# Kernel optimization log

Measured on AMD Instinct MI355X. Metric: run time of the kernel, lower is better.

## Reference

```python
import jax, jax.numpy as jnp
import numpy as np

N, E, H, L, IN, OUT = 50000, 800000, 64, 14, 128, 112
MSG_EPS = 1e-7   # GENConv message epsilon
LN_EPS = 1e-5    # torch.nn.LayerNorm default eps


def setup_inputs() -> dict:
    key = jax.random.key(0)
    ks = jax.random.split(key, 8)
    s = 0.05
    x = jax.random.normal(ks[0], (N, IN), jnp.float32)
    edge_index = jax.random.randint(ks[1], (2, E), 0, N, dtype=jnp.int64)
    enc_W = jax.random.normal(ks[2], (IN, H), jnp.float32) * s
    enc_b = jnp.zeros((H,), jnp.float32)
    ln_g = jnp.ones((L, H), jnp.float32)
    ln_b = jnp.zeros((L, H), jnp.float32)
    mlp_W = jax.random.normal(ks[3], (L, H, H), jnp.float32) * s
    mlp_b = jnp.zeros((L, H), jnp.float32)
    pred_W = jax.random.normal(ks[4], (H, OUT), jnp.float32) * s
    pred_b = jnp.zeros((OUT,), jnp.float32)
    return dict(x=x, edge_index=edge_index, enc_W=enc_W, enc_b=enc_b,
                ln_g=ln_g, ln_b=ln_b, mlp_W=mlp_W, mlp_b=mlp_b,
                pred_W=pred_W, pred_b=pred_b)


def _layernorm(h, g, b):
    mu = jnp.mean(h, axis=-1, keepdims=True)
    var = jnp.mean(jnp.square(h - mu), axis=-1, keepdims=True)  # biased, as torch
    return (h - mu) * jax.lax.rsqrt(var + LN_EPS) * g + b


def _genconv(h, src, dst, W, b):
    # GENConv: msg = relu(x_src) + eps; softmax aggregation (t=1) over dst; out = Linear(x + agg)
    msg = jax.nn.relu(h[src]) + MSG_EPS                    # [E, H]
    mmax = jax.ops.segment_max(msg, dst, num_segments=N)   # [N, H]
    mmax = jnp.where(jnp.isfinite(mmax), mmax, 0.0)         # empty segments
    ex = jnp.exp(msg - mmax[dst])                           # [E, H]
    denom = jax.ops.segment_sum(ex, dst, num_segments=N)    # [N, H]
    num = jax.ops.segment_sum(msg * ex, dst, num_segments=N)
    agg = num / jnp.maximum(denom, 1e-16)                   # 0 for isolated nodes
    return (h + agg) @ W + b


def reference(x, edge_index, enc_W, enc_b, ln_g, ln_b, mlp_W, mlp_b, pred_W, pred_b):
    src, dst = edge_index[0], edge_index[1]
    h = x @ enc_W + enc_b                       # node feature encoder
    h = _genconv(h, src, dst, mlp_W[0], mlp_b[0])  # first GCN (no pre-norm in res+)

    def body(h, params):
        g, bl, W, b = params
        h2 = jax.nn.relu(_layernorm(h, g, bl))  # dropout is identity (eval)
        h = _genconv(h2, src, dst, W, b) + h    # residual
        return h, None

    h, _ = jax.lax.scan(body, h, (ln_g[:L - 1], ln_b[:L - 1], mlp_W[1:], mlp_b[1:]))
    return h @ pred_W + pred_b
```

## Files before the change

kernel.cpp:

```cpp
#include <hip/hip_runtime.h>
#include <hip/hip_bf16.h>

#define NN 50000
#define EE 800000
#define HD 64
#define LL 14
#define IND 128
#define OUTD 112
#define LN2 0.69314718056f

typedef __attribute__((ext_vector_type(8))) short short8;
typedef __attribute__((ext_vector_type(4))) float float4_;
typedef __attribute__((ext_vector_type(4))) unsigned short ushort4_;

__device__ __forceinline__ short bf16_hi(float x) {
    return (short)(__float_as_uint(x) >> 16);
}
__device__ __forceinline__ float bf16_f(short s) {
    return __uint_as_float(((unsigned)(unsigned short)s) << 16);
}
__device__ __forceinline__ float us2f(unsigned u) {
    return __uint_as_float(u << 16);
}
__device__ __forceinline__ unsigned short f2b_rne(float x) {
    unsigned u = __float_as_uint(x);
    u += 0x7fffu + ((u >> 16) & 1u);
    return (unsigned short)(u >> 16);
}

__device__ __forceinline__ void split8(const float* p, short8& hi, short8& lo) {
    float4_ a = *(const float4_*)p;
    float4_ b = *(const float4_*)(p + 4);
    float v[8] = {a[0], a[1], a[2], a[3], b[0], b[1], b[2], b[3]};
    #pragma unroll
    for (int j = 0; j < 8; ++j) {
        short h = bf16_hi(v[j]);
        hi[j] = h;
        lo[j] = bf16_hi(v[j] - bf16_f(h));
    }
}

__device__ __forceinline__ void load_b(const float* __restrict__ W, int ldw,
                                       int colbase, int krow, short8& hi, short8& lo) {
    #pragma unroll
    for (int j = 0; j < 8; ++j) {
        float wv = W[(krow + j) * ldw + colbase];
        short h = bf16_hi(wv);
        hi[j] = h;
        lo[j] = bf16_hi(wv - bf16_f(h));
    }
}

__device__ __forceinline__ float4_ mm3(short8 ah, short8 al, short8 bh, short8 bl,
                                       float4_ acc) {
    acc = __builtin_amdgcn_mfma_f32_16x16x32_bf16(ah, bh, acc, 0, 0, 0);
    acc = __builtin_amdgcn_mfma_f32_16x16x32_bf16(al, bh, acc, 0, 0, 0);
    acc = __builtin_amdgcn_mfma_f32_16x16x32_bf16(ah, bl, acc, 0, 0, 0);
    return acc;
}


__global__ void k_hist(const int* __restrict__ ei, int* __restrict__ cnt,
                       int* __restrict__ rank) {
    int e = blockIdx.x * blockDim.x + threadIdx.x;
    if (e < EE) rank[e] = atomicAdd(&cnt[ei[EE + e]], 1);
}

__global__ __launch_bounds__(1024) void k_scan1(const int* __restrict__ deg,
                                                int* __restrict__ excl,
                                                int* __restrict__ bsum) {
    __shared__ int ws[16];
    int tid = threadIdx.x, lane = tid & 63, w = tid >> 6;
    int gid = blockIdx.x * 1024 + tid;
    int v = (gid < NN) ? deg[gid] : 0;
    int x = v;
    #pragma unroll
    for (int d = 1; d < 64; d <<= 1) {
        int y = __shfl_up(x, d);
        if (lane >= d) x += y;
    }
    if (lane == 63) ws[w] = x;
    __syncthreads();
    if (tid == 0) {
        int acc = 0;
        for (int i = 0; i < 16; i++) { int t = ws[i]; ws[i] = acc; acc += t; }
        bsum[blockIdx.x] = acc;
    }
    __syncthreads();
    if (gid < NN) excl[gid] = x - v + ws[w];
}

__global__ void k_scan2(const int* __restrict__ bsum, int* __restrict__ boff, int nb) {
    int lane = threadIdx.x & 63;
    int v = (lane < nb) ? bsum[lane] : 0;
    int x = v;
    #pragma unroll
    for (int d = 1; d < 64; d <<= 1) {
        int y = __shfl_up(x, d);
        if (lane >= d) x += y;
    }
    if (lane < nb) boff[lane] = x - v;
}

__global__ __launch_bounds__(1024) void k_scan3(int* __restrict__ rp,
                                                const int* __restrict__ boff) {
    int gid = blockIdx.x * 1024 + threadIdx.x;
    if (gid < NN) rp[gid] += boff[blockIdx.x];
    if (gid == 0) rp[NN] = EE;
}

__global__ void k_scatter(const int* __restrict__ ei, const int* __restrict__ rp,
                          const int* __restrict__ rank, int* __restrict__ csrc) {
    int e = blockIdx.x * blockDim.x + threadIdx.x;
    if (e < EE) {
        int d = ei[EE + e];
        csrc[rp[d] + rank[e]] = ei[e];
    }
}


__global__ __launch_bounds__(256) void k_enc(const float* __restrict__ x,
                                             const float* __restrict__ W,
                                             const float* __restrict__ b,
                                             float* __restrict__ h,
                                             unsigned short* __restrict__ P0) {
    __shared__ float X[16 * 132];
    int tid = threadIdx.x, lane = tid & 63, w = tid >> 6;
    int nb = blockIdx.x * 16;
    int nq = lane >> 4, nr = lane & 15;
    int colbase = w * 16 + nr;

    {
        const float* src = x + (size_t)nb * IND + tid * 8;
        float4_ a = *(const float4_*)src;
        float4_ c = *(const float4_*)(src + 4);
        int m = tid >> 4, k8 = 8 * (tid & 15);
        *(float4_*)&X[m * 132 + k8] = a;
        *(float4_*)&X[m * 132 + k8 + 4] = c;
    }
    __syncthreads();

    float4_ acc = {};
    #pragma unroll
    for (int t = 0; t < 4; ++t) {
        short8 ah, al, bh, bl;
        split8(&X[nr * 132 + t * 32 + nq * 8], ah, al);
        load_b(W, HD, colbase, t * 32 + nq * 8, bh, bl);
        acc = mm3(ah, al, bh, bl, acc);
    }

    float bias = b[colbase];
    #pragma unroll
    for (int r = 0; r < 4; ++r) {
        int node = nb + nq * 4 + r;
        float y = acc[r] + bias;
        h[node * HD + colbase] = y;
        float msg = fminf(fmaxf(y, 0.f) + 1e-7f, 50.f);
        P0[node * HD + colbase] = f2b_rne(__expf(msg));
    }
}


__global__ __launch_bounds__(256) void k_gather(const unsigned short* __restrict__ Pin,
                                                const float* __restrict__ selfh,
                                                float* __restrict__ gT,
                                                const int* __restrict__ rp,
                                                const int* __restrict__ csrc) {
    int w = threadIdx.x >> 6, lane = threadIdx.x & 63;
    int node = blockIdx.x * 4 + w;
    int beg = rp[node], deg = rp[node + 1] - beg;

    float s = 0.f, n = 0.f;
    for (int chunk = 0; chunk < deg; chunk += 64) {
        int cnt = min(64, deg - chunk);
        int my = (lane < cnt) ? csrc[beg + chunk + lane] : 0;
        int e = 0;
        for (; e + 4 <= cnt; e += 4) {
            int s0 = __shfl(my, e + 0);
            int s1 = __shfl(my, e + 1);
            int s2 = __shfl(my, e + 2);
            int s3 = __shfl(my, e + 3);
            float p0 = us2f(Pin[s0 * HD + lane]);
            float p1 = us2f(Pin[s1 * HD + lane]);
            float p2 = us2f(Pin[s2 * HD + lane]);
            float p3 = us2f(Pin[s3 * HD + lane]);
            n = fmaf(p0, LN2 * __log2f(p0), n); s += p0;
            n = fmaf(p1, LN2 * __log2f(p1), n); s += p1;
            n = fmaf(p2, LN2 * __log2f(p2), n); s += p2;
            n = fmaf(p3, LN2 * __log2f(p3), n); s += p3;
        }
        for (; e < cnt; ++e) {
            int sr = __shfl(my, e);
            float p = us2f(Pin[sr * HD + lane]);
            n = fmaf(p, LN2 * __log2f(p), n); s += p;
        }
    }
    float agg = n / fmaxf(s, 1e-16f);

    float self;
    if (selfh) {
        self = selfh[(size_t)node * HD + lane];
    } else {
        float ps = us2f(Pin[(size_t)node * HD + lane]);
        self = LN2 * __log2f(ps) - 1e-7f;
    }
    gT[(size_t)node * HD + lane] = self + agg;
}


__global__ __launch_bounds__(256) void k_mm(const float* __restrict__ gT,
                                            const float* __restrict__ hres,
                                            float* __restrict__ hout,
                                            unsigned short* __restrict__ Pout,
                                            const float* __restrict__ W,
                                            const float* __restrict__ b,
                                            const float* __restrict__ gnext,
                                            const float* __restrict__ bnext) {
    __shared__ float T[16 * 68];
    int tid = threadIdx.x, lane = tid & 63, w = tid >> 6;
    int nb = blockIdx.x * 16;
    int nq = lane >> 4, nr = lane & 15;
    int colbase = w * 16 + nr;

    {
        const float* src = gT + (size_t)nb * HD + tid * 4;
        float4_ a = *(const float4_*)src;
        int m = tid >> 4, k4 = 4 * (tid & 15);
        *(float4_*)&T[m * 68 + k4] = a;
    }
    __syncthreads();

    short8 Ahi[2], Alo[2];
    #pragma unroll
    for (int t = 0; t < 2; ++t)
        split8(&T[nr * 68 + t * 32 + nq * 8], Ahi[t], Alo[t]);
    __syncthreads();

    float4_ acc = {};
    #pragma unroll
    for (int t = 0; t < 2; ++t) {
        short8 bh, bl;
        load_b(W, HD, colbase, t * 32 + nq * 8, bh, bl);
        acc = mm3(Ahi[t], Alo[t], bh, bl, acc);
    }

    float bias = b[colbase];
    #pragma unroll
    for (int r = 0; r < 4; ++r) {
        int m = nq * 4 + r;
        int node = nb + m;
        float v = acc[r] + bias;
        if (hres) v += hres[node * HD + colbase];
        hout[node * HD + colbase] = v;
        T[m * 68 + colbase] = v;
    }
    if (!Pout) return;
    __syncthreads();

    int m = tid >> 4, c4 = (tid & 15) * 4;
    float4_ vv = *(const float4_*)&T[m * 68 + c4];
    float ps_ = (vv[0] + vv[1]) + (vv[2] + vv[3]);
    float pq_ = (vv[0] * vv[0] + vv[1] * vv[1]) + (vv[2] * vv[2] + vv[3] * vv[3]);
    #pragma unroll
    for (int d = 8; d; d >>= 1) {
        ps_ += __shfl_xor(ps_, d);
        pq_ += __shfl_xor(pq_, d);
    }
    float mu = ps_ * (1.f / 64.f);
    float var = pq_ * (1.f / 64.f) - mu * mu;
    float inv = rsqrtf(fmaxf(var, 0.f) + 1e-5f);
    float4_ g4 = *(const float4_*)&gnext[c4];
    float4_ b4 = *(const float4_*)&bnext[c4];
    ushort4_ po;
    #pragma unroll
    for (int j = 0; j < 4; ++j) {
        float y = fmaxf((vv[j] - mu) * inv * g4[j] + b4[j], 0.f);
        float msg = fminf(y + 1e-7f, 50.f);
        po[j] = f2b_rne(__expf(msg));
    }
    *(ushort4_*)&Pout[(size_t)(nb + m) * HD + c4] = po;
}


__global__ __launch_bounds__(256) void k_pred(const float* __restrict__ h,
                                              const float* __restrict__ W,
                                              const float* __restrict__ b,
                                              float* __restrict__ out) {
    __shared__ float T[16 * 68];
    int tid = threadIdx.x, lane = tid & 63, w = tid >> 6;
    int nb = blockIdx.x * 16;
    int nq = lane >> 4, nr = lane & 15;

    {
        const float* src = h + (size_t)nb * HD + tid * 4;
        float4_ a = *(const float4_*)src;
        int m = tid >> 4, k4 = 4 * (tid & 15);
        *(float4_*)&T[m * 68 + k4] = a;
    }
    __syncthreads();

    short8 Ahi[2], Alo[2];
    #pragma unroll
    for (int t = 0; t < 2; ++t)
        split8(&T[nr * 68 + t * 32 + nq * 8], Ahi[t], Alo[t]);

    for (int tt = w; tt < 7; tt += 4) {
        int colbase = tt * 16 + nr;
        float4_ acc = {};
        #pragma unroll
        for (int t = 0; t < 2; ++t) {
            short8 bh, bl;
            load_b(W, OUTD, colbase, t * 32 + nq * 8, bh, bl);
            acc = mm3(Ahi[t], Alo[t], bh, bl, acc);
        }
        float bias = b[colbase];
        #pragma unroll
        for (int r = 0; r < 4; ++r) {
            int node = nb + nq * 4 + r;
            out[node * OUTD + colbase] = acc[r] + bias;
        }
    }
}


extern "C" void kernel_launch(void* const* d_in, const int* in_sizes, int n_in,
                              void* d_out, int out_size, void* d_ws, size_t ws_size,
                              hipStream_t stream) {
    const float* x    = (const float*)d_in[0];
    const int*   ei   = (const int*)d_in[1];
    const float* encW = (const float*)d_in[2];
    const float* encb = (const float*)d_in[3];
    const float* lng  = (const float*)d_in[4];
    const float* lnb  = (const float*)d_in[5];
    const float* mlpW = (const float*)d_in[6];
    const float* mlpb = (const float*)d_in[7];
    const float* pW   = (const float*)d_in[8];
    const float* pb   = (const float*)d_in[9];
    float* out = (float*)d_out;

    float* hA  = (float*)d_ws;
    float* hB  = hA + (size_t)NN * HD;
    float* gT  = hB + (size_t)NN * HD;
    unsigned short* PA = (unsigned short*)(gT + (size_t)NN * HD);
    unsigned short* PB = PA + (size_t)NN * HD;
    int* rp    = (int*)(PB + (size_t)NN * HD);
    int* cnt   = rp + (NN + 1);
    int* csrc  = cnt + NN;
    int* rank  = csrc + EE;
    int* bsum  = rank + EE;
    int* boff  = bsum + 64;

    hipMemsetAsync(cnt, 0, NN * sizeof(int), stream);
    k_hist<<<(EE + 255) / 256, 256, 0, stream>>>(ei, cnt, rank);
    const int NB = (NN + 1023) / 1024;
    k_scan1<<<NB, 1024, 0, stream>>>(cnt, rp, bsum);
    k_scan2<<<1, 64, 0, stream>>>(bsum, boff, NB);
    k_scan3<<<NB, 1024, 0, stream>>>(rp, boff);
    k_scatter<<<(EE + 255) / 256, 256, 0, stream>>>(ei, rp, rank, csrc);

    k_enc<<<NN / 16, 256, 0, stream>>>(x, encW, encb, hA, PA);

    k_gather<<<NN / 4, 256, 0, stream>>>(PA, hA, gT, rp, csrc);
    k_mm<<<NN / 16, 256, 0, stream>>>(gT, nullptr, hB, PB,
                                      mlpW, mlpb, lng, lnb);

    float* hres = hB;
    float* hdst = hA;
    unsigned short* pc = PB;
    unsigned short* pn = PA;
    for (int l = 1; l < LL; ++l) {
        bool last = (l == LL - 1);
        k_gather<<<NN / 4, 256, 0, stream>>>(pc, nullptr, gT, rp, csrc);
        k_mm<<<NN / 16, 256, 0, stream>>>(gT, hres, hdst,
                                          last ? nullptr : pn,
                                          mlpW + (size_t)l * HD * HD,
                                          mlpb + (size_t)l * HD,
                                          last ? nullptr : lng + (size_t)l * HD,
                                          last ? nullptr : lnb + (size_t)l * HD);
        float* t = hres; hres = hdst; hdst = t;
        unsigned short* u = pc; pc = pn; pn = u;
    }

    k_pred<<<NN / 16, 256, 0, stream>>>(hres, pW, pb, out);
}
```

Measured before the change: 705.1 us.

## Slice bf16 message table into 8-channel column slabs for cache-local gathers

The exp(message) table is stored as 8 slices of 8 channels per node, so each gather block touches only a 800KB slab that fits better in cache. Each wave now handles 2 nodes, with 8 lanes per edge and 8 edges processed per round, followed by cross-lane reductions. Padding lanes contribute p=1 and are subtracted out through a waste counter. The cost is 8x more blocks, 16-byte per-edge loads (short segments), reloading the CSR indices per slice, and reduction shuffles.

```diff
diff --git a/kernel.cpp b/kernel.cpp
--- a/kernel.cpp
+++ b/kernel.cpp
@@ -150,13 +150,15 @@
     }
 
     float bias = b[colbase];
+    size_t sbase = ((size_t)(colbase >> 3)) * NN;
+    int off = colbase & 7;
     #pragma unroll
     for (int r = 0; r < 4; ++r) {
         int node = nb + nq * 4 + r;
         float y = acc[r] + bias;
         h[node * HD + colbase] = y;
         float msg = fminf(fmaxf(y, 0.f) + 1e-7f, 50.f);
-        P0[node * HD + colbase] = f2b_rne(__expf(msg));
+        P0[(sbase + node) * 8 + off] = f2b_rne(__expf(msg));
     }
 }
 
@@ -167,44 +169,44 @@
                                                 const int* __restrict__ rp,
                                                 const int* __restrict__ csrc) {
     int w = threadIdx.x >> 6, lane = threadIdx.x & 63;
-    int node = blockIdx.x * 4 + w;
-    int beg = rp[node], deg = rp[node + 1] - beg;
-
-    float s = 0.f, n = 0.f;
-    for (int chunk = 0; chunk < deg; chunk += 64) {
-        int cnt = min(64, deg - chunk);
-        int my = (lane < cnt) ? csrc[beg + chunk + lane] : 0;
-        int e = 0;
-        for (; e + 4 <= cnt; e += 4) {
-            int s0 = __shfl(my, e + 0);
-            int s1 = __shfl(my, e + 1);
-            int s2 = __shfl(my, e + 2);
-            int s3 = __shfl(my, e + 3);
-            float p0 = us2f(Pin[s0 * HD + lane]);
-            float p1 = us2f(Pin[s1 * HD + lane]);
-            float p2 = us2f(Pin[s2 * HD + lane]);
-            float p3 = us2f(Pin[s3 * HD + lane]);
-            n = fmaf(p0, LN2 * __log2f(p0), n); s += p0;
-            n = fmaf(p1, LN2 * __log2f(p1), n); s += p1;
-            n = fmaf(p2, LN2 * __log2f(p2), n); s += p2;
-            n = fmaf(p3, LN2 * __log2f(p3), n); s += p3;
-        }
-        for (; e < cnt; ++e) {
-            int sr = __shfl(my, e);
-            float p = us2f(Pin[sr * HD + lane]);
-            n = fmaf(p, LN2 * __log2f(p), n); s += p;
-        }
-    }
-    float agg = n / fmaxf(s, 1e-16f);
-
-    float self;
-    if (selfh) {
-        self = selfh[(size_t)node * HD + lane];
-    } else {
-        float ps = us2f(Pin[(size_t)node * HD + lane]);
-        self = LN2 * __log2f(ps) - 1e-7f;
-    }
-    gT[(size_t)node * HD + lane] = self + agg;
+    int slice = blockIdx.x & 7;
+    int nb = (blockIdx.x >> 3) * 8 + w * 2;
+    int es = lane >> 3, ch = lane & 7;
+    const unsigned short* Ps = Pin + (size_t)slice * NN * 8;
+
+    for (int i = 0; i < 2; ++i) {
+        int node = nb + i;
+        int beg = rp[node];
+        int deg = rp[node + 1] - beg;
+
+        float s = 0.f, n = 0.f;
+        int waste = 0;
+        for (int chunk = 0; chunk < deg; chunk += 64) {
+            int cnt = min(64, deg - chunk);
+            int my = (lane < cnt) ? csrc[beg + chunk + lane] : 0;
+            int rounds = (cnt + 7) >> 3;
+            waste += rounds * 8 - cnt;
+            for (int r = 0; r < rounds; ++r) {
+                int idx = r * 8 + es;
+                int src = __shfl(my, idx);
+                float p = (idx < cnt) ? us2f(Ps[src * 8 + ch]) : 1.0f;
+                n = fmaf(p, __log2f(p), n);
+                s += p;
+            }
+        }
+        #pragma unroll
+        for (int d = 8; d < 64; d <<= 1) {
+            s += __shfl_xor(s, d);
+            n += __shfl_xor(n, d);
+        }
+        if (es == 0) {
+            float agg = LN2 * n / fmaxf(s - (float)waste, 1e-16f);
+            float self;
+            if (selfh) self = selfh[(size_t)node * HD + slice * 8 + ch];
+            else       self = LN2 * __log2f(us2f(Ps[(size_t)node * 8 + ch])) - 1e-7f;
+            gT[(size_t)node * HD + slice * 8 + ch] = self + agg;
+        }
+    }
 }
 
 
@@ -278,7 +280,8 @@
         float msg = fminf(y + 1e-7f, 50.f);
         po[j] = f2b_rne(__expf(msg));
     }
-    *(ushort4_*)&Pout[(size_t)(nb + m) * HD + c4] = po;
+    int slice = c4 >> 3, off = c4 & 7;
+    *(ushort4_*)&Pout[((size_t)slice * NN + (nb + m)) * 8 + off] = po;
 }
 
 
@@ -360,7 +363,9 @@
 
     k_enc<<<NN / 16, 256, 0, stream>>>(x, encW, encb, hA, PA);
 
-    k_gather<<<NN / 4, 256, 0, stream>>>(PA, hA, gT, rp, csrc);
+    const int GB = (NN / 8) * 8;
+
+    k_gather<<<GB, 256, 0, stream>>>(PA, hA, gT, rp, csrc);
     k_mm<<<NN / 16, 256, 0, stream>>>(gT, nullptr, hB, PB,
                                       mlpW, mlpb, lng, lnb);
 
@@ -370,7 +375,7 @@
     unsigned short* pn = PA;
     for (int l = 1; l < LL; ++l) {
         bool last = (l == LL - 1);
-        k_gather<<<NN / 4, 256, 0, stream>>>(pc, nullptr, gT, rp, csrc);
+        k_gather<<<GB, 256, 0, stream>>>(pc, nullptr, gT, rp, csrc);
         k_mm<<<NN / 16, 256, 0, stream>>>(gT, hres, hdst,
                                           last ? nullptr : pn,
                                           mlpW + (size_t)l * HD * HD,
```

Result: slower. 1.600 ms (+126.9%).
